# Kernel optimization log

Measured on AMD Instinct MI355X. Metric: run time of the kernel, lower is better.

The kernel has to match this reference:

```python
import jax, jax.numpy as jnp
import numpy as np

D_MODEL = 1024
NUM_HEADS = 16
DEPTH = D_MODEL // NUM_HEADS


def setup_inputs() -> dict:
    key = jax.random.key(0)
    ks = jax.random.split(key, 9)
    s = 1.0 / np.sqrt(D_MODEL)
    x = jax.random.normal(ks[0], (2, 2048, D_MODEL), dtype=jnp.float32)
    def lin(kw, kb):
        W = jax.random.uniform(kw, (D_MODEL, D_MODEL), jnp.float32, -s, s)
        b = jax.random.uniform(kb, (D_MODEL,), jnp.float32, -s, s)
        return W, b
    Wq, bq = lin(ks[1], ks[2])
    Wk, bk = lin(ks[3], ks[4])
    Wv, bv = lin(ks[5], ks[6])
    Wo, bo = lin(ks[7], ks[8])
    return {"x": x, "Wq": Wq, "bq": bq, "Wk": Wk, "bk": bk,
            "Wv": Wv, "bv": bv, "Wo": Wo, "bo": bo}


def reference(x, Wq, bq, Wk, bk, Wv, bv, Wo, bo):
    B, T, _ = x.shape
    # projections; weights stored as [in, out] (torch Linear applies x @ W.T; here W is already [in,out])
    def split_heads(y):
        return y.reshape(B, T, NUM_HEADS, DEPTH).transpose(0, 2, 1, 3)  # [B,H,T,D]
    Q = split_heads(x @ Wq + bq)
    K = split_heads(x @ Wk + bk)
    V = split_heads(x @ Wv + bv)
    scale = 1.0 / jnp.sqrt(jnp.asarray(DEPTH, dtype=x.dtype))
    scores = jnp.einsum('bhqd,bhkd->bhqk', Q, K) * scale  # [B,H,T,T]
    attn = jax.nn.softmax(scores, axis=-1)
    out = jnp.einsum('bhqk,bhkd->bhqd', attn, V)  # [B,H,T,D]
    out = out.transpose(0, 2, 1, 3).reshape(B, T, D_MODEL)
    return out @ Wo + bo
```

## Files before the change

### kernel.cpp

```cpp
#include <hip/hip_runtime.h>
#include <hip/hip_bf16.h>

typedef unsigned short ushort_t;
typedef short s8v __attribute__((ext_vector_type(8)));
typedef float f4v __attribute__((ext_vector_type(4)));

#define DM 1024
#define TT 2048
#define NH 16
#define DH 64
#define QSCALE 0.18033688011112042f

__device__ __forceinline__ ushort_t f2bf(float f) {
  union { float f; unsigned u; } v; v.f = f;
  unsigned u = v.u;
  return (ushort_t)((u + 0x7fffu + ((u >> 16) & 1u)) >> 16);
}

__device__ __forceinline__ unsigned pk2bf(float a, float b) {
  union { __hip_bfloat162 h; unsigned u; } v;
  v.h = __float22bfloat162_rn(float2{a, b});
  return v.u;
}

__device__ __forceinline__ void gll16(const void* g, const void* l) {
  __builtin_amdgcn_global_load_lds(
      (const __attribute__((address_space(1))) unsigned int*)g,
      (__attribute__((address_space(3))) unsigned int*)l, 16, 0, 0);
}

__global__ __launch_bounds__(256) void wtrans4_kernel(const float* __restrict__ W0,
                                                      const float* __restrict__ W1,
                                                      const float* __restrict__ W2,
                                                      const float* __restrict__ W3,
                                                      ushort_t* __restrict__ dst) {
  __shared__ float tile[32][33];
  const int z = blockIdx.z;
  const float* W = z == 0 ? W0 : (z == 1 ? W1 : (z == 2 ? W2 : W3));
  ushort_t* Wt = dst + (size_t)z * DM * DM;
  int tx = threadIdx.x & 31, ty = threadIdx.x >> 5;
  int n0 = blockIdx.x * 32, k0 = blockIdx.y * 32;
#pragma unroll
  for (int i = 0; i < 4; i++)
    tile[ty + i * 8][tx] = W[(size_t)(k0 + ty + i * 8) * DM + n0 + tx];
  __syncthreads();
#pragma unroll
  for (int i = 0; i < 4; i++)
    Wt[(size_t)(n0 + ty + i * 8) * DM + k0 + tx] = f2bf(tile[tx][ty + i * 8]);
}

__global__ __launch_bounds__(256) void xconv_kernel(const float* __restrict__ x,
                                                    ushort_t* __restrict__ xb) {
  int i = blockIdx.x * 256 + threadIdx.x;
  const float4* p = (const float4*)x + (size_t)i * 2;
  float4 a = p[0], b = p[1];
  union { ushort_t s[8]; uint4 u; } r;
  r.s[0] = f2bf(a.x); r.s[1] = f2bf(a.y); r.s[2] = f2bf(a.z); r.s[3] = f2bf(a.w);
  r.s[4] = f2bf(b.x); r.s[5] = f2bf(b.y); r.s[6] = f2bf(b.z); r.s[7] = f2bf(b.w);
  *((uint4*)xb + i) = r.u;
}

__global__ __launch_bounds__(256) void gemm_bt(
    const ushort_t* __restrict__ A, const ushort_t* __restrict__ Bt, int mode,
    const float* __restrict__ bias0, const float* __restrict__ bias1,
    const float* __restrict__ bias2,
    ushort_t* __restrict__ qo, ushort_t* __restrict__ ko, ushort_t* __restrict__ vo,
    float* __restrict__ co) {
  __shared__ __align__(16) ushort_t Asm[128 * 32];
  __shared__ __align__(16) ushort_t Bsm[128 * 32];
  const int m0 = blockIdx.x * 128, n0 = blockIdx.y * 128;
  const int t = threadIdx.x, lane = t & 63;
  const int wid = t >> 6, wr = wid >> 1, wc = wid & 1;
  const ushort_t* Ab = A + (size_t)m0 * DM;
  const ushort_t* Bb = Bt + (size_t)n0 * DM;

  f4v zero = {0.f, 0.f, 0.f, 0.f};
  f4v acc[4][4];
#pragma unroll
  for (int i = 0; i < 4; i++)
#pragma unroll
    for (int j = 0; j < 4; j++) acc[i][j] = zero;

  const int r0 = t >> 2;
  const int r1 = (t + 256) >> 2;
  const int k8a = (t & 3) * 8;
  const int rr = lane & 15, kk = (lane >> 4) * 8;

  for (int k0 = 0; k0 < DM; k0 += 32) {
    __syncthreads();
    gll16(Ab + (size_t)r0 * DM + k0 + k8a, &Asm[t * 8]);
    gll16(Ab + (size_t)r1 * DM + k0 + k8a, &Asm[(t + 256) * 8]);
    gll16(Bb + (size_t)r0 * DM + k0 + k8a, &Bsm[t * 8]);
    gll16(Bb + (size_t)r1 * DM + k0 + k8a, &Bsm[(t + 256) * 8]);
    asm volatile("s_waitcnt vmcnt(0)" ::: "memory");
    __syncthreads();

    s8v af[4], bf_[4];
#pragma unroll
    for (int mt = 0; mt < 4; mt++)
      af[mt] = *(const s8v*)&Asm[(wr * 64 + mt * 16 + rr) * 32 + kk];
#pragma unroll
    for (int nt = 0; nt < 4; nt++)
      bf_[nt] = *(const s8v*)&Bsm[(wc * 64 + nt * 16 + rr) * 32 + kk];
#pragma unroll
    for (int mt = 0; mt < 4; mt++)
#pragma unroll
      for (int nt = 0; nt < 4; nt++)
        acc[mt][nt] =
            __builtin_amdgcn_mfma_f32_16x16x32_bf16(af[mt], bf_[nt], acc[mt][nt], 0, 0, 0);
  }

  const int col_l = lane & 15, row_q = (lane >> 4) * 4;
  if (mode == 0) {
    const int qkv = n0 >> 10;
    const float* bias = qkv == 0 ? bias0 : (qkv == 1 ? bias1 : bias2);
    ushort_t* dst = qkv == 0 ? qo : (qkv == 1 ? ko : vo);
    const float sc = qkv == 0 ? QSCALE : 1.0f;
    const int nb = n0 & 1023;
#pragma unroll
    for (int nt = 0; nt < 4; nt++) {
      int gc = nb + wc * 64 + nt * 16 + col_l;
      float bv_ = bias[gc];
      int hh = gc >> 6, d = gc & 63;
#pragma unroll
      for (int mt = 0; mt < 4; mt++) {
#pragma unroll
        for (int j = 0; j < 4; j++) {
          int r = m0 + wr * 64 + mt * 16 + row_q + j;
          int bb = r >> 11, tt_ = r & 2047;
          int bhh = bb * NH + hh;
          ushort_t val = f2bf((acc[mt][nt][j] + bv_) * sc);
          if (qkv == 2) {
            dst[((size_t)bhh * DH + d) * TT + tt_] = val;
          } else {
            dst[((size_t)bhh * TT + tt_) * DH + d] = val;
          }
        }
      }
    }
  } else {
#pragma unroll
    for (int nt = 0; nt < 4; nt++) {
      int gc = n0 + wc * 64 + nt * 16 + col_l;
      float bv_ = bias0[gc];
#pragma unroll
      for (int mt = 0; mt < 4; mt++) {
#pragma unroll
        for (int j = 0; j < 4; j++) {
          int r = m0 + wr * 64 + mt * 16 + row_q + j;
          co[(size_t)r * DM + gc] = acc[mt][nt][j] + bv_;
        }
      }
    }
  }
}

__global__ __launch_bounds__(256, 4) void attn_kernel(const ushort_t* __restrict__ Q,
                                                      const ushort_t* __restrict__ K,
                                                      const ushort_t* __restrict__ Vt,
                                                      ushort_t* __restrict__ O) {
  __shared__ __align__(16) ushort_t Ksm[64 * 64];
  __shared__ __align__(16) ushort_t Vsm[64 * 64];
  __shared__ __align__(16) ushort_t Psm[4][16 * 64];

  const int b_lin = blockIdx.x + (blockIdx.y << 5);
  const int xcd = b_lin & 7, n = b_lin >> 3;
  const int bh = (xcd << 2) | (n >> 5);
  const int qt = n & 31;
  const int b = bh >> 4, h = bh & 15;
  const int t = threadIdx.x, lane = t & 63, wid = t >> 6;
  const ushort_t* Qb = Q + ((size_t)bh * TT + qt * 64) * DH;
  const ushort_t* Kb = K + (size_t)bh * TT * DH;
  const ushort_t* Vb = Vt + (size_t)bh * DH * TT;
  const int rr = lane & 15, quad = lane >> 4;
  const int rx = rr & 7;

  s8v qf[2];
#pragma unroll
  for (int kh = 0; kh < 2; kh++)
    qf[kh] = *(const s8v*)&Qb[(size_t)(wid * 16 + rr) * DH + kh * 32 + quad * 8];

  f4v zero = {0.f, 0.f, 0.f, 0.f};
  f4v oacc[4];
  float mreg = -1e30f;
  float lreg = 0.f;
#pragma unroll
  for (int dt = 0; dt < 4; dt++) oacc[dt] = zero;

  ushort_t* Pw = &Psm[wid][0];

  for (int kv0 = 0; kv0 < TT; kv0 += 64) {
    __syncthreads();
#pragma unroll
    for (int c = t; c < 512; c += 256) {
      int row = c >> 3;
      int sch = ((c & 7) ^ (row & 7)) * 8;
      gll16(&Kb[(size_t)(kv0 + row) * DH + sch], &Ksm[c * 8]);
      gll16(&Vb[(size_t)row * TT + kv0 + sch], &Vsm[c * 8]);
    }
    asm volatile("s_waitcnt vmcnt(0)" ::: "memory");
    __syncthreads();

    f4v st[4];
#pragma unroll
    for (int ct = 0; ct < 4; ct++) st[ct] = zero;
    __builtin_amdgcn_s_setprio(1);
#pragma unroll
    for (int ct = 0; ct < 4; ct++) {
      int key = ct * 16 + rr;
#pragma unroll
      for (int kh = 0; kh < 2; kh++) {
        s8v kf = *(const s8v*)&Ksm[key * 64 + (((kh * 4 + quad) ^ (key & 7)) << 3)];
        st[ct] = __builtin_amdgcn_mfma_f32_16x16x32_bf16(kf, qf[kh], st[ct], 0, 0, 0);
      }
    }
    __builtin_amdgcn_s_setprio(0);

    float a0 = fmaxf(fmaxf(st[0][0], st[0][1]), fmaxf(st[0][2], st[0][3]));
    float a1 = fmaxf(fmaxf(st[1][0], st[1][1]), fmaxf(st[1][2], st[1][3]));
    float a2 = fmaxf(fmaxf(st[2][0], st[2][1]), fmaxf(st[2][2], st[2][3]));
    float a3 = fmaxf(fmaxf(st[3][0], st[3][1]), fmaxf(st[3][2], st[3][3]));
    float pmax = fmaxf(fmaxf(a0, a1), fmaxf(a2, a3));
    pmax = fmaxf(pmax, __shfl_xor(pmax, 16, 64));
    pmax = fmaxf(pmax, __shfl_xor(pmax, 32, 64));
    const bool rescale = !__all(pmax <= mreg + 8.0f);
    float corr = 1.0f;
    if (rescale) {
      float mnew = fmaxf(mreg, pmax);
      corr = __builtin_amdgcn_exp2f(mreg - mnew);
      mreg = mnew;
    }
    float ps = 0.f;
#pragma unroll
    for (int ct = 0; ct < 4; ct++) {
#pragma unroll
      for (int j = 0; j < 4; j++) {
        float p = __builtin_amdgcn_exp2f(st[ct][j] - mreg);
        st[ct][j] = p;
        ps += p;
      }
    }
    ps += __shfl_xor(ps, 16, 64);
    ps += __shfl_xor(ps, 32, 64);
    if (rescale) {
      lreg = lreg * corr + ps;
#pragma unroll
      for (int j = 0; j < 4; j++) {
        float cb = __shfl(corr, quad * 4 + j, 64);
#pragma unroll
        for (int dt = 0; dt < 4; dt++) oacc[dt][j] *= cb;
      }
    } else {
      lreg += ps;
    }

#pragma unroll
    for (int ct = 0; ct < 4; ct++) {
      uint2 w;
      w.x = pk2bf(st[ct][0], st[ct][1]);
      w.y = pk2bf(st[ct][2], st[ct][3]);
      int chunk = 2 * ct + (quad >> 1);
      int idx = rr * 64 + ((chunk ^ rx) << 3) + ((quad & 1) << 2);
      *(uint2*)&Pw[idx] = w;
    }
    asm volatile("s_waitcnt lgkmcnt(0)" ::: "memory");
    __builtin_amdgcn_sched_barrier(0);

    __builtin_amdgcn_s_setprio(1);
#pragma unroll
    for (int kh2 = 0; kh2 < 2; kh2++) {
      s8v pa = *(const s8v*)&Pw[rr * 64 + (((kh2 * 4 + quad) ^ rx) << 3)];
#pragma unroll
      for (int dt = 0; dt < 4; dt++) {
        int d = dt * 16 + rr;
        s8v vf = *(const s8v*)&Vsm[d * 64 + (((kh2 * 4 + quad) ^ rx) << 3)];
        oacc[dt] = __builtin_amdgcn_mfma_f32_16x16x32_bf16(pa, vf, oacc[dt], 0, 0, 0);
      }
    }
    __builtin_amdgcn_s_setprio(0);
  }

  float linv = 1.0f / lreg;
#pragma unroll
  for (int j = 0; j < 4; j++) {
    float lb = __shfl(linv, quad * 4 + j, 64);
    int row = qt * 64 + wid * 16 + quad * 4 + j;
#pragma unroll
    for (int dt = 0; dt < 4; dt++) {
      int d = dt * 16 + rr;
      O[((size_t)(b * TT + row)) * DM + h * DH + d] = f2bf(oacc[dt][j] * lb);
    }
  }
}

extern "C" void kernel_launch(void* const* d_in, const int* in_sizes, int n_in,
                              void* d_out, int out_size, void* d_ws, size_t ws_size,
                              hipStream_t stream) {
  const float* x = (const float*)d_in[0];
  const float* Wq = (const float*)d_in[1];
  const float* bq = (const float*)d_in[2];
  const float* Wk = (const float*)d_in[3];
  const float* bk = (const float*)d_in[4];
  const float* Wv = (const float*)d_in[5];
  const float* bv = (const float*)d_in[6];
  const float* Wo = (const float*)d_in[7];
  const float* bo = (const float*)d_in[8];
  float* out = (float*)d_out;

  char* ws = (char*)d_ws;
  ushort_t* xb = (ushort_t*)(ws);
  ushort_t* wqkv = (ushort_t*)(ws + (8ull << 20));
  ushort_t* wot = (ushort_t*)(ws + (14ull << 20));
  ushort_t* Qb = (ushort_t*)(ws + (16ull << 20));
  ushort_t* Kb = (ushort_t*)(ws + (24ull << 20));
  ushort_t* Vtb = (ushort_t*)(ws + (32ull << 20));
  ushort_t* Ob = xb;

  dim3 tb(256);
  wtrans4_kernel<<<dim3(32, 32, 4), tb, 0, stream>>>(Wq, Wk, Wv, Wo, wqkv);
  xconv_kernel<<<dim3(2048), tb, 0, stream>>>(x, xb);
  gemm_bt<<<dim3(32, 24), tb, 0, stream>>>(xb, wqkv, 0, bq, bk, bv, Qb, Kb, Vtb, nullptr);
  attn_kernel<<<dim3(32, 32), tb, 0, stream>>>(Qb, Kb, Vtb, Ob);
  gemm_bt<<<dim3(32, 8), tb, 0, stream>>>(Ob, wot, 1, bo, nullptr, nullptr, nullptr, nullptr,
                                          nullptr, out);
}
```

Before: 233.9 us.

## Double-buffer attention K/V loads, split V transpose, retile output GEMM

The attention kernel now double-buffers its K/V tiles, prefetching the next tile while computing the current one. It also pre-subtracts the running max through the accumulator init and computes max and sum with fewer instructions. The QKV GEMM writes V in head-major layout with coalesced stores, and a separate vtrans kernel produces the transposed V. The output projection GEMM is templated to a 64-row tile so it launches twice as many blocks. These target the exposed load latency in attention, the strided V scatter stores, and low occupancy in the final GEMM, at the cost of an extra launch and double the attention LDS.

```diff
diff --git a/kernel.cpp b/kernel.cpp
--- a/kernel.cpp
+++ b/kernel.cpp
@@ -21,6 +21,10 @@
   union { __hip_bfloat162 h; unsigned u; } v;
   v.h = __float22bfloat162_rn(float2{a, b});
   return v.u;
+}
+
+__device__ __forceinline__ float max3f(float a, float b, float c) {
+  return fmaxf(fmaxf(a, b), c);
 }
 
 __device__ __forceinline__ void gll16(const void* g, const void* l) {
@@ -60,50 +64,76 @@
   *((uint4*)xb + i) = r.u;
 }
 
+__global__ __launch_bounds__(256) void vtrans_kernel(const ushort_t* __restrict__ V,
+                                                     ushort_t* __restrict__ Vt) {
+  __shared__ ushort_t Ls[64][72];
+  const int t = threadIdx.x;
+  const int t0 = blockIdx.x * 64, bh = blockIdx.y;
+  const ushort_t* Vb = V + (size_t)bh * TT * DH;
+  ushort_t* Vtb = Vt + (size_t)bh * DH * TT;
+#pragma unroll
+  for (int c = t; c < 512; c += 256) {
+    int tt = c & 63, dch = c >> 6;
+    union { uint4 u; ushort_t s[8]; } uu;
+    uu.u = *(const uint4*)&Vb[(size_t)(t0 + tt) * DH + dch * 8];
+#pragma unroll
+    for (int i = 0; i < 8; i++) Ls[dch * 8 + i][tt] = uu.s[i];
+  }
+  __syncthreads();
+#pragma unroll
+  for (int c = t; c < 512; c += 256) {
+    int d = c >> 3, tch = c & 7;
+    uint4 u = *(const uint4*)&Ls[d][tch * 8];
+    *(uint4*)&Vtb[(size_t)d * TT + t0 + tch * 8] = u;
+  }
+}
+
+template <int MT, int MODE>
 __global__ __launch_bounds__(256) void gemm_bt(
-    const ushort_t* __restrict__ A, const ushort_t* __restrict__ Bt, int mode,
+    const ushort_t* __restrict__ A, const ushort_t* __restrict__ Bt,
     const float* __restrict__ bias0, const float* __restrict__ bias1,
     const float* __restrict__ bias2,
     ushort_t* __restrict__ qo, ushort_t* __restrict__ ko, ushort_t* __restrict__ vo,
     float* __restrict__ co) {
-  __shared__ __align__(16) ushort_t Asm[128 * 32];
+  constexpr int TM = MT * 32;
+  __shared__ __align__(16) ushort_t Asm[TM * 32];
   __shared__ __align__(16) ushort_t Bsm[128 * 32];
-  const int m0 = blockIdx.x * 128, n0 = blockIdx.y * 128;
+  const int m0 = blockIdx.x * TM, n0 = blockIdx.y * 128;
   const int t = threadIdx.x, lane = t & 63;
   const int wid = t >> 6, wr = wid >> 1, wc = wid & 1;
   const ushort_t* Ab = A + (size_t)m0 * DM;
   const ushort_t* Bb = Bt + (size_t)n0 * DM;
 
   f4v zero = {0.f, 0.f, 0.f, 0.f};
-  f4v acc[4][4];
-#pragma unroll
-  for (int i = 0; i < 4; i++)
+  f4v acc[MT][4];
+#pragma unroll
+  for (int i = 0; i < MT; i++)
 #pragma unroll
     for (int j = 0; j < 4; j++) acc[i][j] = zero;
 
   const int r0 = t >> 2;
-  const int r1 = (t + 256) >> 2;
   const int k8a = (t & 3) * 8;
   const int rr = lane & 15, kk = (lane >> 4) * 8;
 
   for (int k0 = 0; k0 < DM; k0 += 32) {
     __syncthreads();
-    gll16(Ab + (size_t)r0 * DM + k0 + k8a, &Asm[t * 8]);
-    gll16(Ab + (size_t)r1 * DM + k0 + k8a, &Asm[(t + 256) * 8]);
+#pragma unroll
+    for (int p = 0; p < MT / 2; p++)
+      gll16(Ab + (size_t)(r0 + p * 64) * DM + k0 + k8a, &Asm[(t + p * 256) * 8]);
     gll16(Bb + (size_t)r0 * DM + k0 + k8a, &Bsm[t * 8]);
-    gll16(Bb + (size_t)r1 * DM + k0 + k8a, &Bsm[(t + 256) * 8]);
+    gll16(Bb + (size_t)(r0 + 64) * DM + k0 + k8a, &Bsm[(t + 256) * 8]);
     asm volatile("s_waitcnt vmcnt(0)" ::: "memory");
     __syncthreads();
 
-    s8v af[4], bf_[4];
-#pragma unroll
-    for (int mt = 0; mt < 4; mt++)
-      af[mt] = *(const s8v*)&Asm[(wr * 64 + mt * 16 + rr) * 32 + kk];
+    s8v af[MT], bf_[4];
+#pragma unroll
+    for (int mt = 0; mt < MT; mt++)
+      af[mt] = *(const s8v*)&Asm[(wr * (MT * 16) + mt * 16 + rr) * 32 + kk];
 #pragma unroll
     for (int nt = 0; nt < 4; nt++)
       bf_[nt] = *(const s8v*)&Bsm[(wc * 64 + nt * 16 + rr) * 32 + kk];
 #pragma unroll
-    for (int mt = 0; mt < 4; mt++)
+    for (int mt = 0; mt < MT; mt++)
 #pragma unroll
       for (int nt = 0; nt < 4; nt++)
         acc[mt][nt] =
@@ -111,7 +141,7 @@
   }
 
   const int col_l = lane & 15, row_q = (lane >> 4) * 4;
-  if (mode == 0) {
+  if (MODE == 0) {
     const int qkv = n0 >> 10;
     const float* bias = qkv == 0 ? bias0 : (qkv == 1 ? bias1 : bias2);
     ushort_t* dst = qkv == 0 ? qo : (qkv == 1 ? ko : vo);
@@ -123,18 +153,12 @@
       float bv_ = bias[gc];
       int hh = gc >> 6, d = gc & 63;
 #pragma unroll
-      for (int mt = 0; mt < 4; mt++) {
+      for (int mt = 0; mt < MT; mt++) {
 #pragma unroll
         for (int j = 0; j < 4; j++) {
-          int r = m0 + wr * 64 + mt * 16 + row_q + j;
+          int r = m0 + wr * (MT * 16) + mt * 16 + row_q + j;
           int bb = r >> 11, tt_ = r & 2047;
-          int bhh = bb * NH + hh;
-          ushort_t val = f2bf((acc[mt][nt][j] + bv_) * sc);
-          if (qkv == 2) {
-            dst[((size_t)bhh * DH + d) * TT + tt_] = val;
-          } else {
-            dst[((size_t)bhh * TT + tt_) * DH + d] = val;
-          }
+          dst[(((size_t)(bb * NH + hh)) * TT + tt_) * DH + d] = f2bf((acc[mt][nt][j] + bv_) * sc);
         }
       }
     }
@@ -144,10 +168,10 @@
       int gc = n0 + wc * 64 + nt * 16 + col_l;
       float bv_ = bias0[gc];
 #pragma unroll
-      for (int mt = 0; mt < 4; mt++) {
+      for (int mt = 0; mt < MT; mt++) {
 #pragma unroll
         for (int j = 0; j < 4; j++) {
-          int r = m0 + wr * 64 + mt * 16 + row_q + j;
+          int r = m0 + wr * (MT * 16) + mt * 16 + row_q + j;
           co[(size_t)r * DM + gc] = acc[mt][nt][j] + bv_;
         }
       }
@@ -159,8 +183,8 @@
                                                       const ushort_t* __restrict__ K,
                                                       const ushort_t* __restrict__ Vt,
                                                       ushort_t* __restrict__ O) {
-  __shared__ __align__(16) ushort_t Ksm[64 * 64];
-  __shared__ __align__(16) ushort_t Vsm[64 * 64];
+  __shared__ __align__(16) ushort_t Ksm[2][64 * 64];
+  __shared__ __align__(16) ushort_t Vsm[2][64 * 64];
   __shared__ __align__(16) ushort_t Psm[4][16 * 64];
 
   const int b_lin = blockIdx.x + (blockIdx.y << 5);
@@ -182,67 +206,81 @@
 
   f4v zero = {0.f, 0.f, 0.f, 0.f};
   f4v oacc[4];
-  float mreg = -1e30f;
+  float mreg = 0.f;
   float lreg = 0.f;
 #pragma unroll
   for (int dt = 0; dt < 4; dt++) oacc[dt] = zero;
 
+  const int c0r = t >> 3, c0s = ((t & 7) ^ (c0r & 7)) * 8;
+  const int c1 = t + 256;
+  const int c1r = c1 >> 3, c1s = ((t & 7) ^ (c1r & 7)) * 8;
+
+#define STAGE(tv, bb)                                              \
+  do {                                                             \
+    int kv0_ = (tv) * 64;                                          \
+    gll16(&Kb[(size_t)(kv0_ + c0r) * DH + c0s], &Ksm[bb][t * 8]);  \
+    gll16(&Vb[(size_t)c0r * TT + kv0_ + c0s], &Vsm[bb][t * 8]);    \
+    gll16(&Kb[(size_t)(kv0_ + c1r) * DH + c1s], &Ksm[bb][c1 * 8]); \
+    gll16(&Vb[(size_t)c1r * TT + kv0_ + c1s], &Vsm[bb][c1 * 8]);   \
+  } while (0)
+
   ushort_t* Pw = &Psm[wid][0];
 
-  for (int kv0 = 0; kv0 < TT; kv0 += 64) {
-    __syncthreads();
-#pragma unroll
-    for (int c = t; c < 512; c += 256) {
-      int row = c >> 3;
-      int sch = ((c & 7) ^ (row & 7)) * 8;
-      gll16(&Kb[(size_t)(kv0 + row) * DH + sch], &Ksm[c * 8]);
-      gll16(&Vb[(size_t)row * TT + kv0 + sch], &Vsm[c * 8]);
-    }
-    asm volatile("s_waitcnt vmcnt(0)" ::: "memory");
-    __syncthreads();
-
+  STAGE(0, 0);
+  for (int tv = 0; tv < 32; ++tv) {
+    const int cur = tv & 1;
+    if (tv < 31) {
+      STAGE(tv + 1, cur ^ 1);
+      asm volatile("s_waitcnt vmcnt(4)" ::: "memory");
+    } else {
+      asm volatile("s_waitcnt vmcnt(0)" ::: "memory");
+    }
+    __builtin_amdgcn_s_barrier();
+    __builtin_amdgcn_sched_barrier(0);
+
+    f4v minit = {-mreg, -mreg, -mreg, -mreg};
     f4v st[4];
 #pragma unroll
-    for (int ct = 0; ct < 4; ct++) st[ct] = zero;
+    for (int ct = 0; ct < 4; ct++) st[ct] = minit;
     __builtin_amdgcn_s_setprio(1);
 #pragma unroll
     for (int ct = 0; ct < 4; ct++) {
       int key = ct * 16 + rr;
 #pragma unroll
       for (int kh = 0; kh < 2; kh++) {
-        s8v kf = *(const s8v*)&Ksm[key * 64 + (((kh * 4 + quad) ^ (key & 7)) << 3)];
+        s8v kf = *(const s8v*)&Ksm[cur][key * 64 + (((kh * 4 + quad) ^ (key & 7)) << 3)];
         st[ct] = __builtin_amdgcn_mfma_f32_16x16x32_bf16(kf, qf[kh], st[ct], 0, 0, 0);
       }
     }
     __builtin_amdgcn_s_setprio(0);
 
-    float a0 = fmaxf(fmaxf(st[0][0], st[0][1]), fmaxf(st[0][2], st[0][3]));
-    float a1 = fmaxf(fmaxf(st[1][0], st[1][1]), fmaxf(st[1][2], st[1][3]));
-    float a2 = fmaxf(fmaxf(st[2][0], st[2][1]), fmaxf(st[2][2], st[2][3]));
-    float a3 = fmaxf(fmaxf(st[3][0], st[3][1]), fmaxf(st[3][2], st[3][3]));
-    float pmax = fmaxf(fmaxf(a0, a1), fmaxf(a2, a3));
+    float u0 = max3f(st[0][0], st[0][1], st[0][2]);
+    float u1 = max3f(st[0][3], st[1][0], st[1][1]);
+    float u2 = max3f(st[1][2], st[1][3], st[2][0]);
+    float u3 = max3f(st[2][1], st[2][2], st[2][3]);
+    float u4 = max3f(st[3][0], st[3][1], st[3][2]);
+    float pmax = fmaxf(max3f(u0, u1, u2), max3f(u3, u4, st[3][3]));
     pmax = fmaxf(pmax, __shfl_xor(pmax, 16, 64));
     pmax = fmaxf(pmax, __shfl_xor(pmax, 32, 64));
-    const bool rescale = !__all(pmax <= mreg + 8.0f);
-    float corr = 1.0f;
+    float delta = 0.f;
+    const bool rescale = !__all(pmax <= 8.0f);
     if (rescale) {
-      float mnew = fmaxf(mreg, pmax);
-      corr = __builtin_amdgcn_exp2f(mreg - mnew);
-      mreg = mnew;
-    }
-    float ps = 0.f;
+      delta = fmaxf(pmax, 0.0f);
+      mreg += delta;
+#pragma unroll
+      for (int ct = 0; ct < 4; ct++) st[ct] = st[ct] - delta;
+    }
 #pragma unroll
     for (int ct = 0; ct < 4; ct++) {
 #pragma unroll
-      for (int j = 0; j < 4; j++) {
-        float p = __builtin_amdgcn_exp2f(st[ct][j] - mreg);
-        st[ct][j] = p;
-        ps += p;
-      }
-    }
+      for (int j = 0; j < 4; j++) st[ct][j] = __builtin_amdgcn_exp2f(st[ct][j]);
+    }
+    f4v psv = st[0] + st[1] + st[2] + st[3];
+    float ps = (psv[0] + psv[1]) + (psv[2] + psv[3]);
     ps += __shfl_xor(ps, 16, 64);
     ps += __shfl_xor(ps, 32, 64);
     if (rescale) {
+      float corr = __builtin_amdgcn_exp2f(-delta);
       lreg = lreg * corr + ps;
 #pragma unroll
       for (int j = 0; j < 4; j++) {
@@ -273,12 +311,16 @@
 #pragma unroll
       for (int dt = 0; dt < 4; dt++) {
         int d = dt * 16 + rr;
-        s8v vf = *(const s8v*)&Vsm[d * 64 + (((kh2 * 4 + quad) ^ rx) << 3)];
+        s8v vf = *(const s8v*)&Vsm[cur][d * 64 + (((kh2 * 4 + quad) ^ rx) << 3)];
         oacc[dt] = __builtin_amdgcn_mfma_f32_16x16x32_bf16(pa, vf, oacc[dt], 0, 0, 0);
       }
     }
     __builtin_amdgcn_s_setprio(0);
-  }
+
+    __builtin_amdgcn_sched_barrier(0);
+    __builtin_amdgcn_s_barrier();
+  }
+#undef STAGE
 
   float linv = 1.0f / lreg;
 #pragma unroll
@@ -313,14 +355,16 @@
   ushort_t* wot = (ushort_t*)(ws + (14ull << 20));
   ushort_t* Qb = (ushort_t*)(ws + (16ull << 20));
   ushort_t* Kb = (ushort_t*)(ws + (24ull << 20));
-  ushort_t* Vtb = (ushort_t*)(ws + (32ull << 20));
-  ushort_t* Ob = xb;
+  ushort_t* Vb = (ushort_t*)(ws + (32ull << 20));
+  ushort_t* Vtb = xb;
+  ushort_t* Ob = Vb;
 
   dim3 tb(256);
   wtrans4_kernel<<<dim3(32, 32, 4), tb, 0, stream>>>(Wq, Wk, Wv, Wo, wqkv);
   xconv_kernel<<<dim3(2048), tb, 0, stream>>>(x, xb);
-  gemm_bt<<<dim3(32, 24), tb, 0, stream>>>(xb, wqkv, 0, bq, bk, bv, Qb, Kb, Vtb, nullptr);
+  gemm_bt<4, 0><<<dim3(32, 24), tb, 0, stream>>>(xb, wqkv, bq, bk, bv, Qb, Kb, Vb, nullptr);
+  vtrans_kernel<<<dim3(32, 32), tb, 0, stream>>>(Vb, Vtb);
   attn_kernel<<<dim3(32, 32), tb, 0, stream>>>(Qb, Kb, Vtb, Ob);
-  gemm_bt<<<dim3(32, 8), tb, 0, stream>>>(Ob, wot, 1, bo, nullptr, nullptr, nullptr, nullptr,
-                                          nullptr, out);
-}
+  gemm_bt<2, 1><<<dim3(64, 8), tb, 0, stream>>>(Ob, wot, bo, nullptr, nullptr, nullptr, nullptr,
+                                                nullptr, out);
+}
```

Measured after the change: 222.4 us. -4.9%, faster.
